# Kernel tuning notes

Hardware: AMD Instinct MI355X
Metric: run time of the kernel (lower is better)

Reference implementation:

```python
import jax, jax.numpy as jnp
import numpy as np

N = 50000          # nodes
F = 128            # feature dim (indim = outdim)
AVG_DEG = 12       # random edges per node (plus one self-loop)
AVG_D_LOG = 2.6    # avg_d['log'] used by PNA scalers
EPS = 1e-5         # PNA std epsilon / BatchNorm eps


def setup_inputs() -> dict:
    key = jax.random.key(0)
    k1, k2, k3, k4 = jax.random.split(key, 4)
    h = jax.random.normal(k1, (N, F), dtype=jnp.float32)
    E_rand = N * AVG_DEG
    src_r = jax.random.randint(k2, (E_rand,), 0, N)
    dst_r = jax.random.randint(k3, (E_rand,), 0, N)
    loop = jnp.arange(N)
    src = jnp.concatenate([src_r, loop]).astype(jnp.int64) if jax.config.jax_enable_x64 else jnp.concatenate([src_r, loop]).astype(jnp.int32)
    dst = jnp.concatenate([dst_r, loop]).astype(src.dtype)
    concat_dim = F * (1 + 4 * 3)  # indim * (1 + n_aggr * n_scalers)
    W = jax.random.normal(k4, (concat_dim, F), dtype=jnp.float32) * (1.0 / np.sqrt(concat_dim))
    b = jnp.zeros((F,), dtype=jnp.float32)
    gamma = jnp.ones((F,), dtype=jnp.float32)
    beta = jnp.zeros((F,), dtype=jnp.float32)
    return {"h": h, "src": src, "dst": dst, "W": W, "b": b, "gamma": gamma, "beta": beta}


def _pna_forward(h, W, b, gamma, beta, src, dst):
    n = h.shape[0]
    m = h[src]                                            # [E, F] gathered mailbox
    deg = jax.ops.segment_sum(jnp.ones(src.shape[0], h.dtype), dst, num_segments=n)
    deg = jnp.maximum(deg, 1.0)[:, None]                  # every node has a self-loop
    s = jax.ops.segment_sum(m, dst, num_segments=n)
    mean = s / deg
    mx = jax.ops.segment_max(m, dst, num_segments=n)
    mn = jax.ops.segment_min(m, dst, num_segments=n)
    mean_sq = jax.ops.segment_sum(m * m, dst, num_segments=n) / deg
    std = jnp.sqrt(jax.nn.relu(mean_sq - mean * mean) + EPS)
    agg = jnp.concatenate([mean, mx, mn, std], axis=1)    # [N, 4F]
    logd = jnp.log(deg + 1.0)                             # [N, 1]
    scaled = jnp.concatenate([agg,
                              agg * (logd / AVG_D_LOG),
                              agg * (AVG_D_LOG / logd)], axis=1)  # [N, 12F]
    hc = jnp.concatenate([h, scaled], axis=1)             # [N, 13F]
    out = hc @ W + b                                      # posttrans (single linear)
    out = jax.nn.relu(out)                                # activation (dropout p=0)
    mu = out.mean(axis=0)                                 # BatchNorm1d, training stats
    var = out.var(axis=0)                                 # biased variance (torch)
    out = gamma * (out - mu) * jax.lax.rsqrt(var + EPS) + beta
    return out


def reference(h, src, dst, W, b, gamma, beta):
    return _pna_forward(h, W, b, gamma, beta, src, dst)
```

## Files before the change

kernel.cpp:

```cpp
#include <hip/hip_runtime.h>
#include <math.h>

#define FDIM 128
#define AVG_D_LOGF 2.6f
#define BN_EPS 1e-5f
#define NK 10

using f32x4 = __attribute__((ext_vector_type(4))) float;
using s16x8 = __attribute__((ext_vector_type(8))) short;
using u16x8 = __attribute__((ext_vector_type(8))) unsigned short;

__device__ __forceinline__ unsigned short f2bf(float x) {
  unsigned int u = __float_as_uint(x);
  u += 0x7FFFu + ((u >> 16) & 1u);
  return (unsigned short)(u >> 16);
}
__device__ __forceinline__ float bf2f(unsigned short u) {
  return __uint_as_float(((unsigned int)u) << 16);
}

__device__ __forceinline__ void gload16(const void* g, void* l) {
  __builtin_amdgcn_global_load_lds(
      (const __attribute__((address_space(1))) void*)g,
      (__attribute__((address_space(3))) void*)l, 16, 0, 0);
}

__global__ void prep_kernel(const float* __restrict__ h, unsigned short* __restrict__ hb,
                            const float* __restrict__ W, unsigned short* __restrict__ wBT,
                            const int* __restrict__ dst, int* __restrict__ deg,
                            int w0, int w1, int w2, int K) {
  int i = blockIdx.x * 256 + threadIdx.x;
  if (i < w0) {
    const f32x4* sp = (const f32x4*)h + (size_t)i * 2;
    f32x4 v0 = sp[0], v1 = sp[1];
    u16x8 o;
    o[0] = f2bf(v0[0]); o[1] = f2bf(v0[1]); o[2] = f2bf(v0[2]); o[3] = f2bf(v0[3]);
    o[4] = f2bf(v1[0]); o[5] = f2bf(v1[1]); o[6] = f2bf(v1[2]); o[7] = f2bf(v1[3]);
    *((u16x8*)hb + i) = o;
  } else if (i < w0 + w1) {
    int idx = i - w0;
    int k = idx >> 7, j = idx & 127;
    wBT[(size_t)j * K + k] = f2bf(W[idx]);
  } else if (i < w0 + w1 + w2) {
    atomicAdd(&deg[dst[i - w0 - w1]], 1);
  }
}

__global__ void scan1(const int* __restrict__ deg, int* __restrict__ offs,
                      int* __restrict__ bsums, int n) {
  __shared__ int tmp[256];
  int t = threadIdx.x, i = blockIdx.x * 256 + t;
  int v = (i < n) ? deg[i] : 0;
  tmp[t] = v; __syncthreads();
  for (int d = 1; d < 256; d <<= 1) {
    int x = (t >= d) ? tmp[t - d] : 0;
    __syncthreads();
    tmp[t] += x;
    __syncthreads();
  }
  if (i < n) offs[i] = tmp[t] - v;
  if (t == 255) bsums[blockIdx.x] = tmp[255];
}

__global__ void csr_fill(const int* __restrict__ src, const int* __restrict__ dst,
                         const int* __restrict__ offs, const int* __restrict__ bsums,
                         int* __restrict__ cursor, int* __restrict__ csr, int E, int nb) {
  __shared__ int tmp[256];
  __shared__ int ex[256];
  const int t = threadIdx.x;
  {
    int v = (t < nb) ? bsums[t] : 0;
    tmp[t] = v; __syncthreads();
    for (int d = 1; d < 256; d <<= 1) {
      int x = (t >= d) ? tmp[t - d] : 0;
      __syncthreads();
      tmp[t] += x;
      __syncthreads();
    }
    ex[t] = tmp[t] - v;
    __syncthreads();
  }
  int i = blockIdx.x * 256 + t;
  if (i < E) {
    int d = dst[i];
    int pos = offs[d] + ex[d >> 8] + atomicAdd(&cursor[d], 1);
    csr[pos] = src[i];
  }
}

__global__ __launch_bounds__(256) void agg_kernel(
    const unsigned short* __restrict__ hb, const int* __restrict__ csr,
    const int* __restrict__ offs, const int* __restrict__ bsums,
    unsigned short* __restrict__ aggb, float2* __restrict__ s12a,
    int n, int E, int nb) {
  __shared__ int tmp[256];
  __shared__ int ex[256];
  {
    int t = threadIdx.x;
    int v = (t < nb) ? bsums[t] : 0;
    tmp[t] = v; __syncthreads();
    for (int d = 1; d < 256; d <<= 1) {
      int x = (t >= d) ? tmp[t - d] : 0;
      __syncthreads();
      tmp[t] += x;
      __syncthreads();
    }
    ex[t] = tmp[t] - v;
    __syncthreads();
  }
  const int gw = (blockIdx.x * 256 + threadIdx.x) >> 6;
  const int lane = threadIdx.x & 63;
  if (gw >= n) return;
  const int beg = offs[gw] + ex[gw >> 8];
  const int end = (gw + 1 < n) ? offs[gw + 1] + ex[(gw + 1) >> 8] : E;
  const int sub = lane >> 5;
  const int fl  = lane & 31;
  const uint2* hp2 = (const uint2*)hb;

  float s0=0.f,s1=0.f,s2=0.f,s3=0.f, q0=0.f,q1=0.f,q2=0.f,q3=0.f;
  float mx0=-INFINITY,mx1=-INFINITY,mx2=-INFINITY,mx3=-INFINITY;
  float mn0=INFINITY,mn1=INFINITY,mn2=INFINITY,mn3=INFINITY;

  auto acc1 = [&](uint2 A) {
    float a0 = bf2f((unsigned short)A.x), a1 = bf2f((unsigned short)(A.x >> 16));
    float a2 = bf2f((unsigned short)A.y), a3 = bf2f((unsigned short)(A.y >> 16));
    s0 += a0; s1 += a1; s2 += a2; s3 += a3;
    q0 += a0*a0; q1 += a1*a1; q2 += a2*a2; q3 += a3*a3;
    mx0 = fmaxf(mx0,a0); mx1 = fmaxf(mx1,a1); mx2 = fmaxf(mx2,a2); mx3 = fmaxf(mx3,a3);
    mn0 = fminf(mn0,a0); mn1 = fminf(mn1,a1); mn2 = fminf(mn2,a2); mn3 = fminf(mn3,a3);
  };

  const int cnt = end - beg;
  const int pairs = cnt >> 1;
  int p = 0;
  for (; p + 4 <= pairs; p += 4) {
    int base = beg + 2 * p + sub;
    int i0 = csr[base], i1 = csr[base + 2], i2 = csr[base + 4], i3 = csr[base + 6];
    uint2 A = hp2[(size_t)i0 * 32 + fl];
    uint2 B = hp2[(size_t)i1 * 32 + fl];
    uint2 C = hp2[(size_t)i2 * 32 + fl];
    uint2 D = hp2[(size_t)i3 * 32 + fl];
    acc1(A); acc1(B); acc1(C); acc1(D);
  }
  for (; p < pairs; ++p) {
    int i0 = csr[beg + 2 * p + sub];
    acc1(hp2[(size_t)i0 * 32 + fl]);
  }
  if ((cnt & 1) && sub == 0) {
    int i0 = csr[end - 1];
    acc1(hp2[(size_t)i0 * 32 + fl]);
  }

  s0 += __shfl_xor(s0, 32); s1 += __shfl_xor(s1, 32);
  s2 += __shfl_xor(s2, 32); s3 += __shfl_xor(s3, 32);
  q0 += __shfl_xor(q0, 32); q1 += __shfl_xor(q1, 32);
  q2 += __shfl_xor(q2, 32); q3 += __shfl_xor(q3, 32);
  mx0 = fmaxf(mx0, __shfl_xor(mx0, 32)); mx1 = fmaxf(mx1, __shfl_xor(mx1, 32));
  mx2 = fmaxf(mx2, __shfl_xor(mx2, 32)); mx3 = fmaxf(mx3, __shfl_xor(mx3, 32));
  mn0 = fminf(mn0, __shfl_xor(mn0, 32)); mn1 = fminf(mn1, __shfl_xor(mn1, 32));
  mn2 = fminf(mn2, __shfl_xor(mn2, 32)); mn3 = fminf(mn3, __shfl_xor(mn3, 32));

  float degf = (float)cnt;
  if (degf < 1.f) degf = 1.f;
  const float inv = 1.f / degf;
  if (sub == 0) {
    float me0 = s0*inv, me1 = s1*inv, me2 = s2*inv, me3 = s3*inv;
    float st0 = sqrtf(fmaxf(q0*inv - me0*me0, 0.f) + BN_EPS);
    float st1 = sqrtf(fmaxf(q1*inv - me1*me1, 0.f) + BN_EPS);
    float st2 = sqrtf(fmaxf(q2*inv - me2*me2, 0.f) + BN_EPS);
    float st3 = sqrtf(fmaxf(q3*inv - me3*me3, 0.f) + BN_EPS);
    unsigned int b = (unsigned int)gw * 512u + (unsigned int)fl * 4u;
    uint2 wme = make_uint2((unsigned int)f2bf(me0) | ((unsigned int)f2bf(me1) << 16),
                           (unsigned int)f2bf(me2) | ((unsigned int)f2bf(me3) << 16));
    uint2 wmx = make_uint2((unsigned int)f2bf(mx0) | ((unsigned int)f2bf(mx1) << 16),
                           (unsigned int)f2bf(mx2) | ((unsigned int)f2bf(mx3) << 16));
    uint2 wmn = make_uint2((unsigned int)f2bf(mn0) | ((unsigned int)f2bf(mn1) << 16),
                           (unsigned int)f2bf(mn2) | ((unsigned int)f2bf(mn3) << 16));
    uint2 wst = make_uint2((unsigned int)f2bf(st0) | ((unsigned int)f2bf(st1) << 16),
                           (unsigned int)f2bf(st2) | ((unsigned int)f2bf(st3) << 16));
    *(uint2*)&aggb[b      ] = wme;
    *(uint2*)&aggb[b + 128] = wmx;
    *(uint2*)&aggb[b + 256] = wmn;
    *(uint2*)&aggb[b + 384] = wst;
  }
  if (lane == 0) {
    float logd = logf(degf + 1.f);
    s12a[gw] = make_float2(logd / AVG_D_LOGF, AVG_D_LOGF / logd);
  }
}

__global__ __launch_bounds__(256, 3) void gemm_kernel(
    const unsigned short* __restrict__ hb, const unsigned short* __restrict__ wBT,
    const unsigned short* __restrict__ aggb, const float2* __restrict__ s12a,
    const float* __restrict__ bias, float* __restrict__ out,
    float* __restrict__ bnsum, float* __restrict__ bnsq, int n, int K) {
  __shared__ s16x8 As[1024];
  __shared__ s16x8 Bs[3][512];
  const int t = threadIdx.x;
  const int lane = t & 63;
  const int w = t >> 6;
  const int wr = w >> 1, wc = w & 1;
  const int hi = lane >> 4, lr = lane & 15, rx7 = lr & 7;

  const int nwg = gridDim.x;
  const int q = nwg >> 3, r = nwg & 7;
  const int xcd = blockIdx.x & 7, jj = blockIdx.x >> 3;
  const int bx = (xcd < r ? xcd * (q + 1) : r * (q + 1) + (xcd - r) * q) + jj;

  const int m0 = (bx >> 1) * 128;
  const int n0 = (bx & 1) * 64;

  f32x4 acc[3][4][2] = {};

  auto stage = [&](int ss) {
    const bool ph1 = (ss < 2);
    #pragma unroll
    for (int i = 0; i < 4; ++i) {
      int unit = w * 256 + i * 64 + lane;
      int row = unit >> 3, x = unit & 7;
      int node = m0 + row; if (node >= n) node = n - 1;
      int xo = (x ^ (row & 7)) << 3;
      const unsigned short* src = ph1
          ? hb   + (size_t)node * FDIM + ss * 64 + xo
          : aggb + (size_t)node * 512 + (ss - 2) * 64 + xo;
      gload16(src, &As[w * 256 + i * 64]);
    }
    const int nsec = ph1 ? 1 : 3;
    for (int s = 0; s < nsec; ++s) {
      int koff = ph1 ? ss * 64 : (FDIM + s * 512 + (ss - 2) * 64);
      #pragma unroll
      for (int i = 0; i < 2; ++i) {
        int unit = w * 128 + i * 64 + lane;
        int row = unit >> 3, x = unit & 7;
        const unsigned short* src =
            wBT + (size_t)(n0 + row) * K + koff + ((x ^ (row & 7)) << 3);
        gload16(src, &Bs[s][w * 128 + i * 64]);
      }
    }
  };

  for (int step = 0; step < NK; ++step) {
    stage(step);
    __syncthreads();
    #pragma unroll
    for (int ks = 0; ks < 2; ++ks) {
      s16x8 a[4];
      #pragma unroll
      for (int m = 0; m < 4; ++m) {
        int row = wr * 64 + m * 16 + lr;
        a[m] = As[row * 8 + ((ks * 4 + hi) ^ rx7)];
      }
      #pragma unroll
      for (int s = 0; s < 3; ++s) {
        if (step < 2 && s > 0) continue;
        int rb = wc * 32 + lr;
        s16x8 b0 = Bs[s][rb * 8 + ((ks * 4 + hi) ^ rx7)];
        s16x8 b1 = Bs[s][(rb + 16) * 8 + ((ks * 4 + hi) ^ rx7)];
        #pragma unroll
        for (int m = 0; m < 4; ++m) {
          acc[s][m][0] = __builtin_amdgcn_mfma_f32_16x16x32_bf16(a[m], b0, acc[s][m][0], 0, 0, 0);
          acc[s][m][1] = __builtin_amdgcn_mfma_f32_16x16x32_bf16(a[m], b1, acc[s][m][1], 0, 0, 0);
        }
      }
    }
    __syncthreads();
  }

  float* red = (float*)&As[0];
  if (t < 128) red[t] = 0.f;
  __syncthreads();

  const float bv0 = bias[n0 + wc * 32 + lr];
  const float bv1 = bias[n0 + wc * 32 + 16 + lr];
  float cs[2] = {0.f, 0.f}, cq[2] = {0.f, 0.f};
  #pragma unroll
  for (int m = 0; m < 4; ++m) {
    #pragma unroll
    for (int i = 0; i < 4; ++i) {
      int grow = m0 + wr * 64 + m * 16 + hi * 4 + i;
      if (grow >= n) continue;
      float2 sv = s12a[grow];
      #pragma unroll
      for (int nn = 0; nn < 2; ++nn) {
        float v = acc[0][m][nn][i] + sv.x * acc[1][m][nn][i] + sv.y * acc[2][m][nn][i]
                + (nn ? bv1 : bv0);
        v = fmaxf(v, 0.f);
        out[(size_t)grow * FDIM + n0 + wc * 32 + nn * 16 + lr] = v;
        cs[nn] += v; cq[nn] += v * v;
      }
    }
  }
  #pragma unroll
  for (int nn = 0; nn < 2; ++nn) {
    int lc = wc * 32 + nn * 16 + lr;
    atomicAdd(&red[lc], cs[nn]);
    atomicAdd(&red[64 + lc], cq[nn]);
  }
  __syncthreads();
  if (t < 64)       atomicAdd(&bnsum[n0 + t], red[t]);
  else if (t < 128) atomicAdd(&bnsq[n0 + t - 64], red[t]);
}

__global__ void bn_norm(float* __restrict__ out, const float* __restrict__ bnsum,
                        const float* __restrict__ bnsq, const float* __restrict__ gamma,
                        const float* __restrict__ beta, int n) {
  const int j = threadIdx.x & 127;
  const float invN = 1.f / (float)n;
  const float mu = bnsum[j] * invN;
  const float var = bnsq[j] * invN - mu * mu;
  const float rs = rsqrtf(var + BN_EPS);
  const float sc = gamma[j] * rs;
  const float sh = beta[j] - mu * sc;
  const int gt = blockIdx.x * 256 + threadIdx.x;
  const int row0 = gt >> 7;
  const int rstride = (gridDim.x * 256) >> 7;
  for (int i = row0; i < n; i += rstride) {
    size_t idx = (size_t)i * FDIM + j;
    out[idx] = out[idx] * sc + sh;
  }
}

extern "C" void kernel_launch(void* const* d_in, const int* in_sizes, int n_in,
                              void* d_out, int out_size, void* d_ws, size_t ws_size,
                              hipStream_t stream) {
  const float* h     = (const float*)d_in[0];
  const int*   src   = (const int*)d_in[1];
  const int*   dst   = (const int*)d_in[2];
  const float* W     = (const float*)d_in[3];
  const float* bias  = (const float*)d_in[4];
  const float* gamma = (const float*)d_in[5];
  const float* beta  = (const float*)d_in[6];
  float* out = (float*)d_out;

  const int n = in_sizes[0] / FDIM;
  const int E = in_sizes[1];
  const int K = in_sizes[3] / FDIM;

  char* base = (char*)d_ws;
  size_t off = 0;
  auto alloc = [&](size_t bytes) -> void* {
    void* p = base + off;
    off += (bytes + 255) & ~(size_t)255;
    return p;
  };
  int*   deg    = (int*)  alloc(4ull * n);
  int*   cursor = (int*)  alloc(4ull * n);
  float* bnsum  = (float*)alloc(512);
  float* bnsq   = (float*)alloc(512);
  const size_t zlen = off;
  int*    offs  = (int*)  alloc(4ull * (n + 1));
  int*    bsums = (int*)  alloc(4ull * 256);
  int*    csr   = (int*)  alloc(4ull * E);
  float2* s12a  = (float2*)alloc(8ull * n);
  unsigned short* aggb = (unsigned short*)alloc(2ull * (size_t)n * 512);
  unsigned short* wBT  = (unsigned short*)alloc(2ull * (size_t)K * FDIM);
  unsigned short* hb   = (unsigned short*)alloc(2ull * (size_t)n * FDIM);
  (void)ws_size; (void)n_in; (void)out_size;

  const int eb = (E + 255) / 256;
  const int nb = (n + 255) / 256;
  const int w0 = n * FDIM / 8;
  const int w1 = K * FDIM;
  const int w2 = E;

  hipMemsetAsync(d_ws, 0, zlen, stream);
  prep_kernel<<<(w0 + w1 + w2 + 255) / 256, 256, 0, stream>>>(h, hb, W, wBT, dst, deg,
                                                              w0, w1, w2, K);
  scan1<<<nb, 256, 0, stream>>>(deg, offs, bsums, n);
  csr_fill<<<eb, 256, 0, stream>>>(src, dst, offs, bsums, cursor, csr, E, nb);
  agg_kernel<<<(n + 3) / 4, 256, 0, stream>>>(hb, csr, offs, bsums, aggb, s12a, n, E, nb);
  const int gblocks = ((n + 127) / 128) * 2;
  gemm_kernel<<<gblocks, 256, 0, stream>>>(hb, wBT, aggb, s12a, bias,
                                           out, bnsum, bnsq, n, K);
  bn_norm<<<1024, 256, 0, stream>>>(out, bnsum, bnsq, gamma, beta, n);
}
```

Before: 184.1 us.

## Pack aggregation into float2 vectors, raise GEMM occupancy, vectorize BN normalize

Three separate changes. The aggregation accumulators become float2 vectors so the compiler can emit packed FP32 add, multiply, max and min ops, and bf16 pairs are unpacked with two shifts. The GEMM launch bound goes from 3 to 4 waves per SIMD, which may force register spills. The BN normalize kernel now computes scale and shift once per block into shared memory, uses 16-byte vector loads and stores, and launches twice as many blocks.

```diff
diff --git a/kernel.cpp b/kernel.cpp
--- a/kernel.cpp
+++ b/kernel.cpp
@@ -6,6 +6,7 @@
 #define BN_EPS 1e-5f
 #define NK 10
 
+using f32x2 = __attribute__((ext_vector_type(2))) float;
 using f32x4 = __attribute__((ext_vector_type(4))) float;
 using s16x8 = __attribute__((ext_vector_type(8))) short;
 using u16x8 = __attribute__((ext_vector_type(8))) unsigned short;
@@ -17,6 +18,11 @@
 }
 __device__ __forceinline__ float bf2f(unsigned short u) {
   return __uint_as_float(((unsigned int)u) << 16);
+}
+__device__ __forceinline__ f32x2 bfpair(unsigned int u) {
+  union { uint2 u2; f32x2 f; } c;
+  c.u2 = make_uint2(u << 16, u & 0xFFFF0000u);
+  return c.f;
 }
 
 __device__ __forceinline__ void gload16(const void* g, void* l) {
@@ -117,17 +123,19 @@
   const int fl  = lane & 31;
   const uint2* hp2 = (const uint2*)hb;
 
-  float s0=0.f,s1=0.f,s2=0.f,s3=0.f, q0=0.f,q1=0.f,q2=0.f,q3=0.f;
-  float mx0=-INFINITY,mx1=-INFINITY,mx2=-INFINITY,mx3=-INFINITY;
-  float mn0=INFINITY,mn1=INFINITY,mn2=INFINITY,mn3=INFINITY;
+  f32x2 s[2] = {{0.f, 0.f}, {0.f, 0.f}};
+  f32x2 q[2] = {{0.f, 0.f}, {0.f, 0.f}};
+  f32x2 mx[2] = {{-INFINITY, -INFINITY}, {-INFINITY, -INFINITY}};
+  f32x2 mn[2] = {{INFINITY, INFINITY}, {INFINITY, INFINITY}};
 
   auto acc1 = [&](uint2 A) {
-    float a0 = bf2f((unsigned short)A.x), a1 = bf2f((unsigned short)(A.x >> 16));
-    float a2 = bf2f((unsigned short)A.y), a3 = bf2f((unsigned short)(A.y >> 16));
-    s0 += a0; s1 += a1; s2 += a2; s3 += a3;
-    q0 += a0*a0; q1 += a1*a1; q2 += a2*a2; q3 += a3*a3;
-    mx0 = fmaxf(mx0,a0); mx1 = fmaxf(mx1,a1); mx2 = fmaxf(mx2,a2); mx3 = fmaxf(mx3,a3);
-    mn0 = fminf(mn0,a0); mn1 = fminf(mn1,a1); mn2 = fminf(mn2,a2); mn3 = fminf(mn3,a3);
+    f32x2 a0 = bfpair(A.x), a1 = bfpair(A.y);
+    s[0] += a0; s[1] += a1;
+    q[0] += a0 * a0; q[1] += a1 * a1;
+    mx[0] = __builtin_elementwise_max(mx[0], a0);
+    mx[1] = __builtin_elementwise_max(mx[1], a1);
+    mn[0] = __builtin_elementwise_min(mn[0], a0);
+    mn[1] = __builtin_elementwise_min(mn[1], a1);
   };
 
   const int cnt = end - beg;
@@ -151,31 +159,32 @@
     acc1(hp2[(size_t)i0 * 32 + fl]);
   }
 
-  s0 += __shfl_xor(s0, 32); s1 += __shfl_xor(s1, 32);
-  s2 += __shfl_xor(s2, 32); s3 += __shfl_xor(s3, 32);
-  q0 += __shfl_xor(q0, 32); q1 += __shfl_xor(q1, 32);
-  q2 += __shfl_xor(q2, 32); q3 += __shfl_xor(q3, 32);
-  mx0 = fmaxf(mx0, __shfl_xor(mx0, 32)); mx1 = fmaxf(mx1, __shfl_xor(mx1, 32));
-  mx2 = fmaxf(mx2, __shfl_xor(mx2, 32)); mx3 = fmaxf(mx3, __shfl_xor(mx3, 32));
-  mn0 = fminf(mn0, __shfl_xor(mn0, 32)); mn1 = fminf(mn1, __shfl_xor(mn1, 32));
-  mn2 = fminf(mn2, __shfl_xor(mn2, 32)); mn3 = fminf(mn3, __shfl_xor(mn3, 32));
+  #pragma unroll
+  for (int k = 0; k < 2; ++k) {
+    s[k][0] += __shfl_xor(s[k][0], 32);  s[k][1] += __shfl_xor(s[k][1], 32);
+    q[k][0] += __shfl_xor(q[k][0], 32);  q[k][1] += __shfl_xor(q[k][1], 32);
+    mx[k][0] = fmaxf(mx[k][0], __shfl_xor(mx[k][0], 32));
+    mx[k][1] = fmaxf(mx[k][1], __shfl_xor(mx[k][1], 32));
+    mn[k][0] = fminf(mn[k][0], __shfl_xor(mn[k][0], 32));
+    mn[k][1] = fminf(mn[k][1], __shfl_xor(mn[k][1], 32));
+  }
 
   float degf = (float)cnt;
   if (degf < 1.f) degf = 1.f;
   const float inv = 1.f / degf;
   if (sub == 0) {
-    float me0 = s0*inv, me1 = s1*inv, me2 = s2*inv, me3 = s3*inv;
-    float st0 = sqrtf(fmaxf(q0*inv - me0*me0, 0.f) + BN_EPS);
-    float st1 = sqrtf(fmaxf(q1*inv - me1*me1, 0.f) + BN_EPS);
-    float st2 = sqrtf(fmaxf(q2*inv - me2*me2, 0.f) + BN_EPS);
-    float st3 = sqrtf(fmaxf(q3*inv - me3*me3, 0.f) + BN_EPS);
+    f32x2 me0 = s[0] * inv, me1 = s[1] * inv;
+    float st0 = sqrtf(fmaxf(q[0][0] * inv - me0[0] * me0[0], 0.f) + BN_EPS);
+    float st1 = sqrtf(fmaxf(q[0][1] * inv - me0[1] * me0[1], 0.f) + BN_EPS);
+    float st2 = sqrtf(fmaxf(q[1][0] * inv - me1[0] * me1[0], 0.f) + BN_EPS);
+    float st3 = sqrtf(fmaxf(q[1][1] * inv - me1[1] * me1[1], 0.f) + BN_EPS);
     unsigned int b = (unsigned int)gw * 512u + (unsigned int)fl * 4u;
-    uint2 wme = make_uint2((unsigned int)f2bf(me0) | ((unsigned int)f2bf(me1) << 16),
-                           (unsigned int)f2bf(me2) | ((unsigned int)f2bf(me3) << 16));
-    uint2 wmx = make_uint2((unsigned int)f2bf(mx0) | ((unsigned int)f2bf(mx1) << 16),
-                           (unsigned int)f2bf(mx2) | ((unsigned int)f2bf(mx3) << 16));
-    uint2 wmn = make_uint2((unsigned int)f2bf(mn0) | ((unsigned int)f2bf(mn1) << 16),
-                           (unsigned int)f2bf(mn2) | ((unsigned int)f2bf(mn3) << 16));
+    uint2 wme = make_uint2((unsigned int)f2bf(me0[0]) | ((unsigned int)f2bf(me0[1]) << 16),
+                           (unsigned int)f2bf(me1[0]) | ((unsigned int)f2bf(me1[1]) << 16));
+    uint2 wmx = make_uint2((unsigned int)f2bf(mx[0][0]) | ((unsigned int)f2bf(mx[0][1]) << 16),
+                           (unsigned int)f2bf(mx[1][0]) | ((unsigned int)f2bf(mx[1][1]) << 16));
+    uint2 wmn = make_uint2((unsigned int)f2bf(mn[0][0]) | ((unsigned int)f2bf(mn[0][1]) << 16),
+                           (unsigned int)f2bf(mn[1][0]) | ((unsigned int)f2bf(mn[1][1]) << 16));
     uint2 wst = make_uint2((unsigned int)f2bf(st0) | ((unsigned int)f2bf(st1) << 16),
                            (unsigned int)f2bf(st2) | ((unsigned int)f2bf(st3) << 16));
     *(uint2*)&aggb[b      ] = wme;
@@ -189,7 +198,7 @@
   }
 }
 
-__global__ __launch_bounds__(256, 3) void gemm_kernel(
+__global__ __launch_bounds__(256, 4) void gemm_kernel(
     const unsigned short* __restrict__ hb, const unsigned short* __restrict__ wBT,
     const unsigned short* __restrict__ aggb, const float2* __restrict__ s12a,
     const float* __restrict__ bias, float* __restrict__ out,
@@ -304,19 +313,29 @@
 __global__ void bn_norm(float* __restrict__ out, const float* __restrict__ bnsum,
                         const float* __restrict__ bnsq, const float* __restrict__ gamma,
                         const float* __restrict__ beta, int n) {
-  const int j = threadIdx.x & 127;
-  const float invN = 1.f / (float)n;
-  const float mu = bnsum[j] * invN;
-  const float var = bnsq[j] * invN - mu * mu;
-  const float rs = rsqrtf(var + BN_EPS);
-  const float sc = gamma[j] * rs;
-  const float sh = beta[j] - mu * sc;
-  const int gt = blockIdx.x * 256 + threadIdx.x;
-  const int row0 = gt >> 7;
-  const int rstride = (gridDim.x * 256) >> 7;
-  for (int i = row0; i < n; i += rstride) {
-    size_t idx = (size_t)i * FDIM + j;
-    out[idx] = out[idx] * sc + sh;
+  __shared__ float scs[128], shs[128];
+  const int t = threadIdx.x;
+  if (t < 128) {
+    const float invN = 1.f / (float)n;
+    const float mu = bnsum[t] * invN;
+    const float var = bnsq[t] * invN - mu * mu;
+    const float rs = rsqrtf(var + BN_EPS);
+    const float s = gamma[t] * rs;
+    scs[t] = s; shs[t] = beta[t] - mu * s;
+  }
+  __syncthreads();
+  const int total = n * 32;
+  int idx = blockIdx.x * 256 + t;
+  const int c4 = (idx & 31) * 4;
+  const float s0 = scs[c4], s1 = scs[c4 + 1], s2 = scs[c4 + 2], s3 = scs[c4 + 3];
+  const float h0 = shs[c4], h1 = shs[c4 + 1], h2 = shs[c4 + 2], h3 = shs[c4 + 3];
+  for (; idx < total; idx += gridDim.x * 256) {
+    f32x4 v = ((f32x4*)out)[idx];
+    v[0] = v[0] * s0 + h0;
+    v[1] = v[1] * s1 + h1;
+    v[2] = v[2] * s2 + h2;
+    v[3] = v[3] * s3 + h3;
+    ((f32x4*)out)[idx] = v;
   }
 }
 
@@ -372,5 +391,5 @@
   const int gblocks = ((n + 127) / 128) * 2;
   gemm_kernel<<<gblocks, 256, 0, stream>>>(hb, wBT, aggb, s12a, bias,
                                            out, bnsum, bnsq, n, K);
-  bn_norm<<<1024, 256, 0, stream>>>(out, bnsum, bnsq, gamma, beta, n);
-}
+  bn_norm<<<2048, 256, 0, stream>>>(out, bnsum, bnsq, gamma, beta, n);
+}
```

New measurement: 211.8 us. 1.15x slower.
